# Optimization experiments

Measured on AMD Instinct MI355X. Metric: run time of the kernel, lower is better.

## Reference

```python
import jax, jax.numpy as jnp
import numpy as np

K = 5
K2 = K * K  # 25
SLOPE = 0.01  # torch leaky_relu default


def _unfold(x, k):
    # torch.nn.Unfold(k) on reflect-padded x: channel order c-major, then kh, kw
    b, c, h, w = x.shape
    p = k // 2
    xp = jnp.pad(x, ((0, 0), (0, 0), (p, p), (p, p)), mode='reflect')
    cols = jnp.stack([xp[:, :, i:i + h, j:j + w] for i in range(k) for j in range(k)], axis=2)
    return cols.reshape(b, c * k * k, h * w)  # (b, 3*k^2, h*w)


def _lin(x, W, b):
    # torch Linear: W is (out, in)
    return x @ W.T + b


def _lrelu(x):
    return jnp.where(x >= 0, x, SLOPE * x)


def setup_inputs() -> dict:
    key = jax.random.key(0)
    ks = iter(jax.random.split(key, 64))
    d = {}
    d['x'] = jax.random.uniform(next(ks), (4, 3, 384, 384), dtype=jnp.float32)

    def mk(name, out_f, in_f):
        d['W_' + name] = jax.random.normal(next(ks), (out_f, in_f), jnp.float32) * (1.0 / np.sqrt(in_f))
        d['b_' + name] = jax.random.normal(next(ks), (out_f,), jnp.float32) * 0.01

    mk('input', 2 * K2, 3 * K2)
    mk('h1', 3 * K2, 2 * K2)
    mk('h2', 3 * K2, 3 * K2)
    mk('h3', 2 * K2, 2 * K2)
    mk('h4', 5 * K2, 2 * K2)
    mk('h5', 2 * K2, 5 * K2)
    mk('out', 3, 2 * K2)
    # encoder(3*k^2): in -> 3*in -> in -> 3
    mk('e1', 9 * K2, 3 * K2); mk('e2', 3 * K2, 9 * K2); mk('e3', 3, 3 * K2)
    # encoder(2*k^2)
    mk('f1', 6 * K2, 2 * K2); mk('f2', 2 * K2, 6 * K2); mk('f3', 3, 2 * K2)
    # decoder(2*k^2): 3 -> out -> 3*out -> out
    mk('d1', 2 * K2, 3); mk('d2', 6 * K2, 2 * K2); mk('d3', 2 * K2, 6 * K2)
    return d


def reference(x,
              W_input, b_input, W_h1, b_h1, W_h2, b_h2, W_h3, b_h3,
              W_h4, b_h4, W_h5, b_h5, W_out, b_out,
              W_e1, b_e1, W_e2, b_e2, W_e3, b_e3,
              W_f1, b_f1, W_f2, b_f2, W_f3, b_f3,
              W_d1, b_d1, W_d2, b_d2, W_d3, b_d3):
    b, c, h, w = x.shape
    sw = jnp.transpose(_unfold(x, K), (0, 2, 1))  # (b, h*w, 3*k^2)
    x1 = _lin(sw, W_input, b_input)
    x2 = _lrelu(_lin(x1, W_h1, b_h1))
    x3 = jnp.tanh(_lin(x2, W_h2, b_h2))
    x3_enc = _lin(_lin(_lin(x3, W_e1, b_e1), W_e2, b_e2), W_e3, b_e3)
    enc2_x1 = _lin(_lin(_lin(x1, W_f1, b_f1), W_f2, b_f2), W_f3, b_f3)
    x4 = _lrelu(x3_enc + enc2_x1)
    x4_dec = _lin(_lin(_lin(_lin(x4, W_d1, b_d1), W_d2, b_d2), W_d3, b_d3), W_h3, b_h3)
    x5 = jnp.tanh(_lin(x4_dec, W_h4, b_h4))
    x6 = _lin(x5, W_h5, b_h5) - x1
    x7 = _lrelu(_lin(x6, W_out, b_out))  # (b, h*w, 3)
    return jnp.transpose(x7, (0, 2, 1)).reshape(b, c, h, w)
```

## Files before the change

kernel.cpp:

```cpp
#include <hip/hip_runtime.h>


#define IW 384
#define HW (384 * 384)
#define NPIX (4 * HW)
#define MTILE 128
#define NBLK (NPIX / MTILE)
#define AST 68

typedef _Float16 half8 __attribute__((ext_vector_type(8)));
typedef __fp16 fp16x2 __attribute__((ext_vector_type(2)));
typedef __attribute__((ext_vector_type(4))) float f32x4;
typedef __attribute__((ext_vector_type(4))) unsigned int uint4_;

#define MFMAH(A, B, C) __builtin_amdgcn_mfma_f32_16x16x32_f16((A), (B), (C), 0, 0, 0)

#define BA   0
#define B1   64
#define B2   144
#define BEF  224
#define BD   240
#define B4   304
#define B5   432
#define BOUT 496
#define BIAS_TOT 512

#define W_A0   0
#define W_A1   2048
#define W_A2   4096
#define W_H1A  6144
#define W_H1B  8704
#define W_H2A  11264
#define W_H2B  13824
#define W_H2C  16384
#define W_EF   18944
#define W_D    24064
#define W_H4C0 28160
#define W_H5C0 30208
#define W_OUT  44544
#define W_NI   45568
#define W_TOT  47616

#define STG_BE  24320
#define STG_BF  24336

__device__ __forceinline__ float lrelu(float v) { return v >= 0.0f ? v : 0.01f * v; }

__device__ __forceinline__ float tanh_fast(float v) {
    float e = __expf(2.0f * v);
    return 1.0f - 2.0f * __builtin_amdgcn_rcpf(e + 1.0f);
}

__device__ __forceinline__ unsigned short f2h_bits(float v) {
    union { _Float16 h; unsigned short s; } u; u.h = (_Float16)v; return u.s;
}
__device__ __forceinline__ float h2f_bits(unsigned short s) {
    union { _Float16 h; unsigned short s; } u; u.s = s; return (float)u.h;
}
__device__ __forceinline__ unsigned packh2(float a, float b) {
    union { fp16x2 h; unsigned u; } u;
    u.h = __builtin_amdgcn_cvt_pkrtz(a, b);
    return u.u;
}

__device__ __forceinline__ void stage(float* dst, const float* __restrict__ src,
                                      int n, int tid) {
    int n4 = n >> 2;
    float4* d = (float4*)dst;
    const float4* s = (const float4*)src;
#pragma unroll 4
    for (int i = tid; i < n4; i += 256) d[i] = s[i];
    for (int i = (n4 << 2) + tid; i < n; i += 256) dst[i] = src[i];
}

__global__ __launch_bounds__(256) void setup_all(
    const float* __restrict__ W_input, const float* __restrict__ b_input,
    const float* __restrict__ W_h1,  const float* __restrict__ b_h1,
    const float* __restrict__ W_h2,  const float* __restrict__ b_h2,
    const float* __restrict__ W_h3,  const float* __restrict__ b_h3,
    const float* __restrict__ W_h4,  const float* __restrict__ b_h4,
    const float* __restrict__ W_h5,  const float* __restrict__ b_h5,
    const float* __restrict__ W_out, const float* __restrict__ b_out,
    const float* __restrict__ W_e1,  const float* __restrict__ b_e1,
    const float* __restrict__ W_e2,  const float* __restrict__ b_e2,
    const float* __restrict__ W_e3,  const float* __restrict__ b_e3,
    const float* __restrict__ W_f1,  const float* __restrict__ b_f1,
    const float* __restrict__ W_f2,  const float* __restrict__ b_f2,
    const float* __restrict__ W_f3,  const float* __restrict__ b_f3,
    const float* __restrict__ W_d1,  const float* __restrict__ b_d1,
    const float* __restrict__ W_d2,  const float* __restrict__ b_d2,
    const float* __restrict__ W_d3,  const float* __restrict__ b_d3,
    float* __restrict__ ws)
{
    const int tid = threadIdx.x;
    const int NT = 256;
    short* wimg = (short*)(ws + BIAS_TOT);

    if (blockIdx.x < 71) {
        const int soff[17] = {W_A0,W_A1,W_A2, W_H1A,W_H1B, W_H2A,W_H2B,W_H2C,
                              W_H4C0,W_H5C0, W_H4C0+4096,W_H5C0+4096,
                              W_H4C0+8192,W_H5C0+8192, W_H4C0+12288,W_H5C0+12288,
                              W_OUT};
        const int slay[17] = {0,0,0, 1,1, 2,2,2, 6,7, 6,7, 6,7, 6,7, 8};
        const int sNT[17]  = {4,4,4, 5,5, 5,5,5, 2,4, 2,4, 2,4, 2,4, 1};
        const int sKTS[17] = {1,1,1, 1,1, 1,1,1, 2,1, 2,1, 2,1, 2,1, 2};
        const int snb[17]  = {0,0,0, 0,0, 0,0,0, 0,0, 32,0, 64,0, 96,0, 0};
        const int skb[17]  = {0,32,64, 0,32, 0,32,64, 0,0, 0,32, 0,64, 0,96, 0};

        int seg = 0, local = blockIdx.x;
        while (seg < 16 && local >= sNT[seg] * sKTS[seg]) { local -= sNT[seg] * sKTS[seg]; seg++; }
        const int kts = sKTS[seg];
        const int kt = local % kts, nt = local / kts;
        const int lay = slay[seg];
        short* dst = wimg + soff[seg] + local * 512;

#pragma unroll
        for (int t = 0; t < 2; t++) {
            int idx = tid + t * 256;
            int j = idx & 7, lane = idx >> 3;
            int n = snb[seg] + nt * 16 + (lane & 15);
            int k = skb[seg] + kt * 32 + (lane >> 4) * 8 + j;
            float v = 0.0f;
            switch (lay) {
                case 0: if (n < 50  && k < 75)  v = W_input[n * 75 + k]; break;
                case 1: if (n < 75  && k < 50)  v = W_h1[n * 50 + k]; break;
                case 2: if (n < 75  && k < 75)  v = W_h2[n * 75 + k]; break;
                case 6: if (n < 125 && k < 50)  v = W_h4[n * 50 + k]; break;
                case 7: if (n < 50  && k < 125) v = W_h5[n * 125 + k]; break;
                case 8: if (n < 3   && k < 50)  v = W_out[n * 50 + k]; break;
            }
            dst[idx] = (short)f2h_bits(v);
        }
        return;
    }

    if (blockIdx.x == 74) {
        for (int i = tid; i < BIAS_TOT; i += NT) {
            if (i >= BD && i < B4) continue;
            float v = 0.0f;
            if (i < B1)        { int o = i - BA;   if (o < 50)  v = b_input[o]; }
            else if (i < B2)   { int o = i - B1;   if (o < 75)  v = b_h1[o]; }
            else if (i < BEF)  { int o = i - B2;   if (o < 75)  v = b_h2[o]; }
            else if (i < BD)   { v = 0.0f; }
            else if (i < B5)   { int o = i - B4;   if (o < 125) v = b_h4[o]; }
            else if (i < BOUT) { int o = i - B5;   if (o < 50)  v = b_h5[o]; }
            else               { int o = i - BOUT; if (o < 3)   v = b_out[o]; }
            ws[i] = v;
        }
        for (int i = tid; i < 2048; i += NT) {
            int j = i & 7, lane = (i >> 3) & 63, nt = i >> 9;
            int n = nt * 16 + (lane & 15);
            int k = (nt >> 1) * 32 + (lane >> 4) * 8 + j;
            wimg[W_NI + i] = (short)f2h_bits(k == n ? -1.0f : 0.0f);
        }
        return;
    }

    __shared__ __align__(16) float A[17500];
    __shared__ float B[675];
    __shared__ float C[256];
    __shared__ float Dd[256];
    __shared__ float Es[256];
    __shared__ float S[232];

    if (blockIdx.x == 71) {
        stage(A, W_e2, 16875, tid);
        for (int i = tid; i < 225; i += NT) { Es[i] = W_e3[i]; C[i] = b_e1[i]; }
        __syncthreads();
        for (int o = tid; o < 675; o += NT) {
            int r = o / 225, c = o % 225;
            float s0 = 0.f, s1 = 0.f, s2 = 0.f;
#pragma unroll
            for (int t = 0; t < 75; t += 3) {
                s0 += Es[r * 75 + t]     * A[t * 225 + c];
                s1 += Es[r * 75 + t + 1] * A[(t + 1) * 225 + c];
                s2 += Es[r * 75 + t + 2] * A[(t + 2) * 225 + c];
            }
            B[o] = s0 + s1 + s2;
        }
        for (int o = tid; o < 75; o += NT) {
            float s0 = 0.f, s1 = 0.f, s2 = 0.f;
#pragma unroll
            for (int t = 0; t < 225; t += 3) {
                s0 += A[o * 225 + t]     * C[t];
                s1 += A[o * 225 + t + 1] * C[t + 1];
                s2 += A[o * 225 + t + 2] * C[t + 2];
            }
            Dd[o] = b_e2[o] + s0 + s1 + s2;
        }
        __syncthreads();
        stage(A, W_e1, 16875, tid);
        __syncthreads();
        for (int o = tid; o < 225; o += NT) {
            int r = o / 75, c = o % 75;
            float s0 = 0.f, s1 = 0.f, s2 = 0.f;
#pragma unroll
            for (int t = 0; t < 225; t += 3) {
                s0 += B[r * 225 + t]     * A[t * 75 + c];
                s1 += B[r * 225 + t + 1] * A[(t + 1) * 75 + c];
                s2 += B[r * 225 + t + 2] * A[(t + 2) * 75 + c];
            }
            S[o] = s0 + s1 + s2;
        }
        for (int o = tid; o < 16; o += NT) {
            float s = 0.0f;
            if (o < 3) {
                s = b_e3[o];
                for (int t = 0; t < 75; t++) s += Es[o * 75 + t] * Dd[t];
            }
            ws[STG_BE + o] = s;
        }
        __syncthreads();
        for (int i = tid; i < 3072; i += NT) {
            int j = i & 7, lane = (i >> 3) & 63, frag = i >> 9, pl = frag & 1, kt = frag >> 1;
            int n = lane & 15, k = kt * 32 + (lane >> 4) * 8 + j;
            float v = (n < 3 && k < 75) ? S[n * 75 + k] : 0.0f;
            float hi = h2f_bits(f2h_bits(v));
            wimg[W_EF + i] = (short)(pl ? f2h_bits(v - hi) : f2h_bits(v));
        }
    } else if (blockIdx.x == 72) {
        stage(A,        W_f2, 7500, tid);
        stage(A + 7500, W_f1, 7500, tid);
        for (int i = tid; i < 150; i += NT) { Es[i] = W_f3[i]; C[i] = b_f1[i]; }
        __syncthreads();
        for (int o = tid; o < 450; o += NT) {
            int r = o / 150, c = o % 150;
            float s0 = 0.f, s1 = 0.f;
#pragma unroll
            for (int t = 0; t < 50; t += 2) {
                s0 += Es[r * 50 + t]     * A[t * 150 + c];
                s1 += Es[r * 50 + t + 1] * A[(t + 1) * 150 + c];
            }
            B[o] = s0 + s1;
        }
        for (int o = tid; o < 50; o += NT) {
            float s0 = 0.f, s1 = 0.f;
#pragma unroll
            for (int t = 0; t < 150; t += 2) {
                s0 += A[o * 150 + t]     * C[t];
                s1 += A[o * 150 + t + 1] * C[t + 1];
            }
            Dd[o] = b_f2[o] + s0 + s1;
        }
        __syncthreads();
        for (int o = tid; o < 150; o += NT) {
            int r = o / 50, c = o % 50;
            float s0 = 0.f, s1 = 0.f;
#pragma unroll
            for (int t = 0; t < 150; t += 2) {
                s0 += B[r * 150 + t]     * A[7500 + t * 50 + c];
                s1 += B[r * 150 + t + 1] * A[7500 + (t + 1) * 50 + c];
            }
            S[o] = s0 + s1;
        }
        for (int o = tid; o < 16; o += NT) {
            float s = 0.0f;
            if (o < 3) {
                s = b_f3[o];
                for (int t = 0; t < 50; t++) s += Es[o * 50 + t] * Dd[t];
            }
            ws[STG_BF + o] = s;
        }
        __syncthreads();
        for (int i = tid; i < 2048; i += NT) {
            int j = i & 7, lane = (i >> 3) & 63, frag = i >> 9, pl = frag & 1, kt = frag >> 1;
            int n = lane & 15, k = kt * 32 + (lane >> 4) * 8 + j;
            float v = (n < 3 && k < 50) ? S[n * 50 + k] : 0.0f;
            float hi = h2f_bits(f2h_bits(v));
            wimg[W_EF + 3072 + i] = (short)(pl ? f2h_bits(v - hi) : f2h_bits(v));
        }
    } else {
        stage(A,         W_d2, 7500, tid);
        stage(A + 7500,  W_d3, 7500, tid);
        stage(A + 15000, W_h3, 2500, tid);
        for (int i = tid; i < 150; i += NT) Es[i] = W_d1[i];
        for (int i = tid; i < 50;  i += NT) C[i] = b_d1[i];
        __syncthreads();
        for (int o = tid; o < 450; o += NT) {
            int r = o / 3, c = o % 3;
            float s0 = 0.f, s1 = 0.f;
#pragma unroll
            for (int t = 0; t < 50; t += 2) {
                s0 += A[r * 50 + t]     * Es[t * 3 + c];
                s1 += A[r * 50 + t + 1] * Es[(t + 1) * 3 + c];
            }
            B[o] = s0 + s1;
        }
        for (int o = tid; o < 150; o += NT) {
            float s0 = 0.f, s1 = 0.f;
#pragma unroll
            for (int t = 0; t < 50; t += 2) {
                s0 += A[o * 50 + t]     * C[t];
                s1 += A[o * 50 + t + 1] * C[t + 1];
            }
            Dd[o] = b_d2[o] + s0 + s1;
        }
        __syncthreads();
        for (int o = tid; o < 150; o += NT) {
            int r = o / 3, c = o % 3;
            float s0 = 0.f, s1 = 0.f;
#pragma unroll
            for (int t = 0; t < 150; t += 2) {
                s0 += A[7500 + r * 150 + t]     * B[t * 3 + c];
                s1 += A[7500 + r * 150 + t + 1] * B[(t + 1) * 3 + c];
            }
            Es[o] = s0 + s1;
        }
        for (int o = tid; o < 50; o += NT) {
            float s0 = 0.f, s1 = 0.f;
#pragma unroll
            for (int t = 0; t < 150; t += 2) {
                s0 += A[7500 + o * 150 + t]     * Dd[t];
                s1 += A[7500 + o * 150 + t + 1] * Dd[t + 1];
            }
            C[o] = b_d3[o] + s0 + s1;
        }
        __syncthreads();
        for (int o = tid; o < 150; o += NT) {
            int r = o / 3, c = o % 3;
            float s0 = 0.f, s1 = 0.f;
#pragma unroll
            for (int t = 0; t < 50; t += 2) {
                s0 += A[15000 + r * 50 + t]     * Es[t * 3 + c];
                s1 += A[15000 + r * 50 + t + 1] * Es[(t + 1) * 3 + c];
            }
            S[o] = s0 + s1;
        }
        for (int o = tid; o < 64; o += NT) {
            float v = 0.0f;
            if (o < 50) {
                float s0 = 0.f, s1 = 0.f;
#pragma unroll
                for (int t = 0; t < 50; t += 2) {
                    s0 += A[15000 + o * 50 + t]     * C[t];
                    s1 += A[15000 + o * 50 + t + 1] * C[t + 1];
                }
                v = b_h3[o] + s0 + s1;
            }
            ws[BD + o] = v;
        }
        __syncthreads();
        for (int i = tid; i < 4096; i += NT) {
            int j = i & 7, lane = (i >> 3) & 63, frag = i >> 9, pl = frag & 1, nt = frag >> 1;
            int n = nt * 16 + (lane & 15), k = (lane >> 4) * 8 + j;
            float v = (n < 50 && k < 3) ? S[n * 3 + k] : 0.0f;
            float hi = h2f_bits(f2h_bits(v));
            wimg[W_D + i] = (short)(pl ? f2h_bits(v - hi) : f2h_bits(v));
        }
    }
}

__device__ __forceinline__ half8 gfragH(const short* __restrict__ wl, int off) {
    return *(const half8*)(wl + off);
}

__device__ __forceinline__ half8 readAf(const unsigned int* acts, int row0, int pane, int lane) {
    int m = lane & 15, qd = lane >> 4;
    const unsigned int* p = &acts[(row0 + m) * AST + pane + (qd & 1) * 8];
    uint4_ a = *(const uint4_*)p;
    uint4_ b = *(const uint4_*)(p + 4);
    unsigned sel = (qd >> 1) ? 0x07060302u : 0x05040100u;
    union { unsigned u[4]; half8 v; } r;
    r.u[0] = __builtin_amdgcn_perm(a.y, a.x, sel);
    r.u[1] = __builtin_amdgcn_perm(a.w, a.z, sel);
    r.u[2] = __builtin_amdgcn_perm(b.y, b.x, sel);
    r.u[3] = __builtin_amdgcn_perm(b.w, b.z, sel);
    return r.v;
}

__device__ __forceinline__ void writeCf(unsigned int* acts, int row0q, int dcol,
                                        f32x4 va, f32x4 vb) {
    unsigned int* p = &acts[row0q * AST + dcol];
#pragma unroll
    for (int r = 0; r < 4; r++) p[r * AST] = packh2(va[r], vb[r]);
}

__device__ __forceinline__ void t2s(f32x4& a0, f32x4& a1, half8 x0, half8 x1, half8 b) {
    a0 = MFMAH(x0, b, a0);
    a1 = MFMAH(x1, b, a1);
}
__device__ __forceinline__ void t2p(f32x4& a0, f32x4& a1, half8 x0, half8 x1,
                                    half8 bh, half8 bl) {
    a0 = MFMAH(x0, bh, a0);
    a1 = MFMAH(x1, bh, a1);
    a0 = MFMAH(x0, bl, a0);
    a1 = MFMAH(x1, bl, a1);
}

__global__ __launch_bounds__(256, 4) void fused_mfma(
    const float* __restrict__ xin,
    const float* __restrict__ ws,
    float* __restrict__ out)
{
    __shared__ unsigned int acts[MTILE * AST];

    const int tid = threadIdx.x;
    const int wv = tid >> 6;
    const int lane = tid & 63;
    const int qd = lane >> 4;
    const int mcol = lane & 15;
    const int rw = wv * 32;
    const short* __restrict__ wl = (const short*)(ws + BIAS_TOT) + lane * 8;
    const f32x4 zero4 = {0.f, 0.f, 0.f, 0.f};

    const int g0 = blockIdx.x * MTILE;
    const int bb = g0 / HW;
    const int p0 = g0 - bb * HW;
    const int yb = p0 / IW;
    const int xblk = p0 - yb * IW;
    const float* __restrict__ xb = xin + bb * 3 * HW;

    float* patch = (float*)acts;
    int*   stab  = (int*)(acts + 1984);

    for (int e = tid; e < 1980; e += 256) {
        int cr = e / 132;
        int i  = e - cr * 132;
        int c  = cr / 5, r = cr - c * 5;
        int ty = yb + r - 2; ty = ty < 0 ? -ty : ty; ty = (766 - ty) < ty ? 766 - ty : ty;
        int tx = xblk - 2 + i; tx = tx < 0 ? -tx : tx; tx = (766 - tx) < tx ? 766 - tx : tx;
        patch[cr * 132 + i] = xb[c * HW + ty * IW + tx];
    }
    if (tid < 96) {
        int v = 0;
        if (tid < 75) {
            int c = tid / 25, rem = tid - 25 * c;
            int rr = rem / 5, ss = rem - 5 * rr;
            v = (c * 5 + rr) * 132 + ss;
        }
        stab[tid] = v;
    }
    __syncthreads();

    half8 swf[3][2];
    {
        int st[3][8];
#pragma unroll
        for (int kt = 0; kt < 3; kt++)
#pragma unroll
            for (int j = 0; j < 8; j++)
                st[kt][j] = stab[kt * 32 + qd * 8 + j];
#pragma unroll
        for (int mt = 0; mt < 2; mt++) {
            const int xloc = wv * 32 + mt * 16 + mcol;
#pragma unroll
            for (int kt = 0; kt < 3; kt++) {
                union { unsigned u32[4]; half8 v; } u;
#pragma unroll
                for (int jj = 0; jj < 8; jj += 2) {
                    float v0 = patch[st[kt][jj]     + xloc];
                    float v1 = patch[st[kt][jj + 1] + xloc];
                    if (kt == 2) {
                        int qq0 = 64 + qd * 8 + jj;
                        v0 = (qq0     < 75) ? v0 : 0.0f;
                        v1 = (qq0 + 1 < 75) ? v1 : 0.0f;
                    }
                    u.u32[jj >> 1] = packh2(v0, v1);
                }
                swf[kt][mt] = u.v;
            }
        }
    }
    __syncthreads();

    f32x4 accA[4][2];
#pragma unroll
    for (int nt = 0; nt < 4; nt++) { accA[nt][0] = zero4; accA[nt][1] = zero4; }
#pragma unroll
    for (int nt = 0; nt < 4; nt++)
        t2s(accA[nt][0], accA[nt][1], swf[0][0], swf[0][1], gfragH(wl, W_A0 + nt * 512));
#pragma unroll
    for (int nt = 0; nt < 4; nt++)
        t2s(accA[nt][0], accA[nt][1], swf[1][0], swf[1][1], gfragH(wl, W_A1 + nt * 512));
#pragma unroll
    for (int nt = 0; nt < 4; nt++)
        t2s(accA[nt][0], accA[nt][1], swf[2][0], swf[2][1], gfragH(wl, W_A2 + nt * 512));

    half8 x1f[2][2];
#pragma unroll
    for (int nt = 0; nt < 4; nt++) {
        float bv = ws[BA + nt * 16 + mcol];
#pragma unroll
        for (int mt = 0; mt < 2; mt++) {
            accA[nt][mt][0] += bv; accA[nt][mt][1] += bv;
            accA[nt][mt][2] += bv; accA[nt][mt][3] += bv;
        }
    }
#pragma unroll
    for (int mt = 0; mt < 2; mt++) {
        writeCf(acts, rw + mt * 16 + qd * 4, mcol,      accA[0][mt], accA[1][mt]);
        writeCf(acts, rw + mt * 16 + qd * 4, 16 + mcol, accA[2][mt], accA[3][mt]);
    }
#pragma unroll
    for (int kt = 0; kt < 2; kt++)
#pragma unroll
        for (int mt = 0; mt < 2; mt++)
            x1f[kt][mt] = readAf(acts, rw + mt * 16, kt * 16, lane);

    f32x4 acc1[5][2];
#pragma unroll
    for (int nt = 0; nt < 5; nt++) { acc1[nt][0] = zero4; acc1[nt][1] = zero4; }
#pragma unroll
    for (int nt = 0; nt < 5; nt++)
        t2s(acc1[nt][0], acc1[nt][1], x1f[0][0], x1f[0][1], gfragH(wl, W_H1A + nt * 512));
#pragma unroll
    for (int nt = 0; nt < 5; nt++)
        t2s(acc1[nt][0], acc1[nt][1], x1f[1][0], x1f[1][1], gfragH(wl, W_H1B + nt * 512));
#pragma unroll
    for (int mt = 0; mt < 2; mt++) {
        f32x4 w5[5];
#pragma unroll
        for (int nt = 0; nt < 5; nt++) {
            float bv = ws[B1 + nt * 16 + mcol];
            f32x4 v = acc1[nt][mt];
            v[0] = lrelu(v[0] + bv); v[1] = lrelu(v[1] + bv);
            v[2] = lrelu(v[2] + bv); v[3] = lrelu(v[3] + bv);
            w5[nt] = v;
        }
        writeCf(acts, rw + mt * 16 + qd * 4, mcol,      w5[0], w5[1]);
        writeCf(acts, rw + mt * 16 + qd * 4, 16 + mcol, w5[2], w5[3]);
        writeCf(acts, rw + mt * 16 + qd * 4, 32 + mcol, w5[4], zero4);
    }

    f32x4 acc2[5][2];
#pragma unroll
    for (int nt = 0; nt < 5; nt++) { acc2[nt][0] = zero4; acc2[nt][1] = zero4; }
    {
        half8 a0 = readAf(acts, rw, 0, lane), a1 = readAf(acts, rw + 16, 0, lane);
#pragma unroll
        for (int nt = 0; nt < 5; nt++)
            t2s(acc2[nt][0], acc2[nt][1], a0, a1, gfragH(wl, W_H2A + nt * 512));
    }
    {
        half8 a0 = readAf(acts, rw, 16, lane), a1 = readAf(acts, rw + 16, 16, lane);
#pragma unroll
        for (int nt = 0; nt < 5; nt++)
            t2s(acc2[nt][0], acc2[nt][1], a0, a1, gfragH(wl, W_H2B + nt * 512));
    }
    {
        half8 a0 = readAf(acts, rw, 32, lane), a1 = readAf(acts, rw + 16, 32, lane);
#pragma unroll
        for (int nt = 0; nt < 5; nt++)
            t2s(acc2[nt][0], acc2[nt][1], a0, a1, gfragH(wl, W_H2C + nt * 512));
    }
#pragma unroll
    for (int mt = 0; mt < 2; mt++) {
        f32x4 w5[5];
#pragma unroll
        for (int nt = 0; nt < 5; nt++) {
            float bv = ws[B2 + nt * 16 + mcol];
            f32x4 v = acc2[nt][mt];
            v[0] = tanh_fast(v[0] + bv); v[1] = tanh_fast(v[1] + bv);
            v[2] = tanh_fast(v[2] + bv); v[3] = tanh_fast(v[3] + bv);
            w5[nt] = v;
        }
        writeCf(acts, rw + mt * 16 + qd * 4, mcol,      w5[0], w5[1]);
        writeCf(acts, rw + mt * 16 + qd * 4, 16 + mcol, w5[2], w5[3]);
        writeCf(acts, rw + mt * 16 + qd * 4, 32 + mcol, w5[4], zero4);
    }

    f32x4 accEF[2];
    {
        float bv = ws[STG_BE + mcol] + ws[STG_BF + mcol];
        accEF[0] = (f32x4){bv, bv, bv, bv};
        accEF[1] = accEF[0];
    }
#pragma unroll
    for (int kt = 0; kt < 3; kt++) {
        half8 a0 = readAf(acts, rw, kt * 16, lane), a1 = readAf(acts, rw + 16, kt * 16, lane);
        t2p(accEF[0], accEF[1], a0, a1,
            gfragH(wl, W_EF + kt * 1024), gfragH(wl, W_EF + kt * 1024 + 512));
    }
#pragma unroll
    for (int kt = 0; kt < 2; kt++)
        t2p(accEF[0], accEF[1], x1f[kt][0], x1f[kt][1],
            gfragH(wl, W_EF + 3072 + kt * 1024), gfragH(wl, W_EF + 3072 + kt * 1024 + 512));
    half8 x4f[2];
#pragma unroll
    for (int mt = 0; mt < 2; mt++) {
        f32x4 v = accEF[mt];
        v[0] = lrelu(v[0]); v[1] = lrelu(v[1]); v[2] = lrelu(v[2]); v[3] = lrelu(v[3]);
        writeCf(acts, rw + mt * 16 + qd * 4, 32 + mcol, v, zero4);
    }
    x4f[0] = readAf(acts, rw, 32, lane);
    x4f[1] = readAf(acts, rw + 16, 32, lane);

    f32x4 accD[4][2];
#pragma unroll
    for (int nt = 0; nt < 4; nt++) {
        float bv = ws[BD + nt * 16 + mcol];
        accD[nt][0] = (f32x4){bv, bv, bv, bv};
        accD[nt][1] = accD[nt][0];
    }
#pragma unroll
    for (int nt = 0; nt < 4; nt++)
        t2p(accD[nt][0], accD[nt][1], x4f[0], x4f[1],
            gfragH(wl, W_D + nt * 1024), gfragH(wl, W_D + nt * 1024 + 512));
#pragma unroll
    for (int mt = 0; mt < 2; mt++) {
        writeCf(acts, rw + mt * 16 + qd * 4, mcol,      accD[0][mt], accD[1][mt]);
        writeCf(acts, rw + mt * 16 + qd * 4, 16 + mcol, accD[2][mt], accD[3][mt]);
    }
    half8 xdf[2][2];
#pragma unroll
    for (int kt = 0; kt < 2; kt++)
#pragma unroll
        for (int mt = 0; mt < 2; mt++)
            xdf[kt][mt] = readAf(acts, rw + mt * 16, kt * 16, lane);

    f32x4 x6a[4][2];
#pragma unroll
    for (int nt = 0; nt < 4; nt++) {
        float bv = ws[B5 + nt * 16 + mcol];
        half8 nI = gfragH(wl, W_NI + nt * 512);
#pragma unroll
        for (int mt = 0; mt < 2; mt++) {
            f32x4 v = {bv, bv, bv, bv};
            x6a[nt][mt] = MFMAH(x1f[nt >> 1][mt], nI, v);
        }
    }

#pragma unroll
    for (int c = 0; c < 4; c++) {
        const int slot = 32 + (c & 1) * 16;
        f32x4 acc5[2][2];
#pragma unroll
        for (int nt2 = 0; nt2 < 2; nt2++) {
            float bv = ws[B4 + c * 32 + nt2 * 16 + mcol];
            acc5[nt2][0] = (f32x4){bv, bv, bv, bv};
            acc5[nt2][1] = acc5[nt2][0];
        }
#pragma unroll
        for (int nt2 = 0; nt2 < 2; nt2++)
#pragma unroll
            for (int kt = 0; kt < 2; kt++)
                t2s(acc5[nt2][0], acc5[nt2][1], xdf[kt][0], xdf[kt][1],
                    gfragH(wl, W_H4C0 + c * 4096 + (nt2 * 2 + kt) * 512));
#pragma unroll
        for (int mt = 0; mt < 2; mt++) {
            f32x4 v0 = acc5[0][mt], v1 = acc5[1][mt];
            v0[0] = tanh_fast(v0[0]); v0[1] = tanh_fast(v0[1]);
            v0[2] = tanh_fast(v0[2]); v0[3] = tanh_fast(v0[3]);
            v1[0] = tanh_fast(v1[0]); v1[1] = tanh_fast(v1[1]);
            v1[2] = tanh_fast(v1[2]); v1[3] = tanh_fast(v1[3]);
            writeCf(acts, rw + mt * 16 + qd * 4, slot + mcol, v0, v1);
        }
        half8 chf[2];
        chf[0] = readAf(acts, rw, slot, lane);
        chf[1] = readAf(acts, rw + 16, slot, lane);
#pragma unroll
        for (int nt = 0; nt < 4; nt++)
            t2s(x6a[nt][0], x6a[nt][1], chf[0], chf[1],
                gfragH(wl, W_H5C0 + c * 4096 + nt * 512));
    }

#pragma unroll
    for (int mt = 0; mt < 2; mt++) {
        writeCf(acts, rw + mt * 16 + qd * 4, mcol,      x6a[0][mt], x6a[1][mt]);
        writeCf(acts, rw + mt * 16 + qd * 4, 16 + mcol, x6a[2][mt], x6a[3][mt]);
    }
    f32x4 accO[2];
    {
        float bv = ws[BOUT + mcol];
        accO[0] = (f32x4){bv, bv, bv, bv};
        accO[1] = accO[0];
    }
#pragma unroll
    for (int kt = 0; kt < 2; kt++) {
        half8 a0 = readAf(acts, rw, kt * 16, lane), a1 = readAf(acts, rw + 16, kt * 16, lane);
        t2s(accO[0], accO[1], a0, a1, gfragH(wl, W_OUT + kt * 512));
    }
    if (mcol < 3) {
#pragma unroll
        for (int mt = 0; mt < 2; mt++) {
#pragma unroll
            for (int r = 0; r < 4; r++) {
                int p = p0 + wv * 32 + mt * 16 + qd * 4 + r;
                out[(bb * 3 + mcol) * HW + p] = lrelu(accO[mt][r]);
            }
        }
    }
}

extern "C" void kernel_launch(void* const* d_in, const int* in_sizes, int n_in,
                              void* d_out, int out_size, void* d_ws, size_t ws_size,
                              hipStream_t stream)
{
    const float* xin = (const float*)d_in[0];
    float* ws = (float*)d_ws;

    setup_all<<<75, 256, 0, stream>>>(
        (const float*)d_in[1],  (const float*)d_in[2],
        (const float*)d_in[3],  (const float*)d_in[4],
        (const float*)d_in[5],  (const float*)d_in[6],
        (const float*)d_in[7],  (const float*)d_in[8],
        (const float*)d_in[9],  (const float*)d_in[10],
        (const float*)d_in[11], (const float*)d_in[12],
        (const float*)d_in[13], (const float*)d_in[14],
        (const float*)d_in[15], (const float*)d_in[16],
        (const float*)d_in[17], (const float*)d_in[18],
        (const float*)d_in[19], (const float*)d_in[20],
        (const float*)d_in[21], (const float*)d_in[22],
        (const float*)d_in[23], (const float*)d_in[24],
        (const float*)d_in[25], (const float*)d_in[26],
        (const float*)d_in[27], (const float*)d_in[28],
        (const float*)d_in[29], (const float*)d_in[30],
        (const float*)d_in[31], (const float*)d_in[32],
        ws);

    fused_mfma<<<NBLK, 256, 0, stream>>>(xin, ws, (float*)d_out);
}
```

Before: 226.5 us.

## Transpose MFMA operand roles so activations round-trip LDS with vector stores

Swaps the MFMA operand order so weights are the A operand and pixel activations the B operand. Each lane then owns contiguous output features for one pixel, which lets intermediate activations be written as packed 64-bit stores and read back as 128-bit loads without byte permutes. Biases are loaded as vectors into the accumulator initialisation, the LDS row stride shrinks, and occupancy hints rise to 6 blocks. tanh now uses exp2 with a folded constant and lrelu uses fmax. This relies on the weight image layout being valid for the transposed operand role, and on padding being zeroed correctly after the masking for the third K tile was removed.

```diff
diff --git a/kernel.cpp b/kernel.cpp
--- a/kernel.cpp
+++ b/kernel.cpp
@@ -6,12 +6,13 @@
 #define NPIX (4 * HW)
 #define MTILE 128
 #define NBLK (NPIX / MTILE)
-#define AST 68
+#define NST 52
+#define PT16 (16 * NST)
 
 typedef _Float16 half8 __attribute__((ext_vector_type(8)));
 typedef __fp16 fp16x2 __attribute__((ext_vector_type(2)));
 typedef __attribute__((ext_vector_type(4))) float f32x4;
-typedef __attribute__((ext_vector_type(4))) unsigned int uint4_;
+typedef __attribute__((ext_vector_type(2))) unsigned int uint2_;
 
 #define MFMAH(A, B, C) __builtin_amdgcn_mfma_f32_16x16x32_f16((A), (B), (C), 0, 0, 0)
 
@@ -44,11 +45,17 @@
 #define STG_BE  24320
 #define STG_BF  24336
 
-__device__ __forceinline__ float lrelu(float v) { return v >= 0.0f ? v : 0.01f * v; }
+__device__ __forceinline__ float lrelu(float v) { return fmaxf(v, 0.01f * v); }
+
+#if __has_builtin(__builtin_amdgcn_exp2f)
+#define EXP2F __builtin_amdgcn_exp2f
+#else
+#define EXP2F __builtin_exp2f
+#endif
 
 __device__ __forceinline__ float tanh_fast(float v) {
-    float e = __expf(2.0f * v);
-    return 1.0f - 2.0f * __builtin_amdgcn_rcpf(e + 1.0f);
+    float e = EXP2F(v * 2.8853900817779268f);
+    return __builtin_fmaf(-2.0f, __builtin_amdgcn_rcpf(e + 1.0f), 1.0f);
 }
 
 __device__ __forceinline__ unsigned short f2h_bits(float v) {
@@ -354,54 +361,36 @@
     return *(const half8*)(wl + off);
 }
 
-__device__ __forceinline__ half8 readAf(const unsigned int* acts, int row0, int pane, int lane) {
-    int m = lane & 15, qd = lane >> 4;
-    const unsigned int* p = &acts[(row0 + m) * AST + pane + (qd & 1) * 8];
-    uint4_ a = *(const uint4_*)p;
-    uint4_ b = *(const uint4_*)(p + 4);
-    unsigned sel = (qd >> 1) ? 0x07060302u : 0x05040100u;
-    union { unsigned u[4]; half8 v; } r;
-    r.u[0] = __builtin_amdgcn_perm(a.y, a.x, sel);
-    r.u[1] = __builtin_amdgcn_perm(a.w, a.z, sel);
-    r.u[2] = __builtin_amdgcn_perm(b.y, b.x, sel);
-    r.u[3] = __builtin_amdgcn_perm(b.w, b.z, sel);
-    return r.v;
-}
-
-__device__ __forceinline__ void writeCf(unsigned int* acts, int row0q, int dcol,
-                                        f32x4 va, f32x4 vb) {
-    unsigned int* p = &acts[row0q * AST + dcol];
-#pragma unroll
-    for (int r = 0; r < 4; r++) p[r * AST] = packh2(va[r], vb[r]);
-}
-
-__device__ __forceinline__ void t2s(f32x4& a0, f32x4& a1, half8 x0, half8 x1, half8 b) {
-    a0 = MFMAH(x0, b, a0);
-    a1 = MFMAH(x1, b, a1);
-}
-__device__ __forceinline__ void t2p(f32x4& a0, f32x4& a1, half8 x0, half8 x1,
-                                    half8 bh, half8 bl) {
-    a0 = MFMAH(x0, bh, a0);
-    a1 = MFMAH(x1, bh, a1);
-    a0 = MFMAH(x0, bl, a0);
-    a1 = MFMAH(x1, bl, a1);
-}
-
-__global__ __launch_bounds__(256, 4) void fused_mfma(
+__device__ __forceinline__ void wB(unsigned int* p, f32x4 v) {
+    uint2_ u;
+    u[0] = packh2(v[0], v[1]);
+    u[1] = packh2(v[2], v[3]);
+    *(uint2_*)p = u;
+}
+
+__device__ __forceinline__ f32x4 lrelu4(f32x4 v) {
+    v[0] = lrelu(v[0]); v[1] = lrelu(v[1]); v[2] = lrelu(v[2]); v[3] = lrelu(v[3]);
+    return v;
+}
+__device__ __forceinline__ f32x4 tanh4(f32x4 v) {
+    v[0] = tanh_fast(v[0]); v[1] = tanh_fast(v[1]);
+    v[2] = tanh_fast(v[2]); v[3] = tanh_fast(v[3]);
+    return v;
+}
+
+__global__ __launch_bounds__(256, 6) void fused_mfma(
     const float* __restrict__ xin,
     const float* __restrict__ ws,
     float* __restrict__ out)
 {
-    __shared__ unsigned int acts[MTILE * AST];
+    __shared__ unsigned int acts[MTILE * NST];
 
     const int tid = threadIdx.x;
     const int wv = tid >> 6;
     const int lane = tid & 63;
     const int qd = lane >> 4;
     const int mcol = lane & 15;
-    const int rw = wv * 32;
     const short* __restrict__ wl = (const short*)(ws + BIAS_TOT) + lane * 8;
-    const f32x4 zero4 = {0.f, 0.f, 0.f, 0.f};
 
     const int g0 = blockIdx.x * MTILE;
     const int bb = g0 / HW;
@@ -441,8 +430,8 @@
             for (int j = 0; j < 8; j++)
                 st[kt][j] = stab[kt * 32 + qd * 8 + j];
 #pragma unroll
-        for (int mt = 0; mt < 2; mt++) {
-            const int xloc = wv * 32 + mt * 16 + mcol;
+        for (int pt = 0; pt < 2; pt++) {
+            const int xloc = wv * 32 + pt * 16 + mcol;
 #pragma unroll
             for (int kt = 0; kt < 3; kt++) {
                 union { unsigned u32[4]; half8 v; } u;
@@ -450,234 +439,213 @@
                 for (int jj = 0; jj < 8; jj += 2) {
                     float v0 = patch[st[kt][jj]     + xloc];
                     float v1 = patch[st[kt][jj + 1] + xloc];
-                    if (kt == 2) {
-                        int qq0 = 64 + qd * 8 + jj;
-                        v0 = (qq0     < 75) ? v0 : 0.0f;
-                        v1 = (qq0 + 1 < 75) ? v1 : 0.0f;
-                    }
                     u.u32[jj >> 1] = packh2(v0, v1);
                 }
-                swf[kt][mt] = u.v;
+                swf[kt][pt] = u.v;
             }
         }
     }
     __syncthreads();
 
+    unsigned int* myrow = acts + (wv * 32 + mcol) * NST;
+    unsigned int* wp = myrow + 2 * qd;
+    const unsigned int* rp = myrow + 4 * qd;
+
+    {
+        uint2_ z; z[0] = 0u; z[1] = 0u;
+        *(uint2_*)(wp + 40) = z;
+        *(uint2_*)(wp + PT16 + 40) = z;
+    }
+
     f32x4 accA[4][2];
 #pragma unroll
-    for (int nt = 0; nt < 4; nt++) { accA[nt][0] = zero4; accA[nt][1] = zero4; }
-#pragma unroll
-    for (int nt = 0; nt < 4; nt++)
-        t2s(accA[nt][0], accA[nt][1], swf[0][0], swf[0][1], gfragH(wl, W_A0 + nt * 512));
-#pragma unroll
-    for (int nt = 0; nt < 4; nt++)
-        t2s(accA[nt][0], accA[nt][1], swf[1][0], swf[1][1], gfragH(wl, W_A1 + nt * 512));
-#pragma unroll
-    for (int nt = 0; nt < 4; nt++)
-        t2s(accA[nt][0], accA[nt][1], swf[2][0], swf[2][1], gfragH(wl, W_A2 + nt * 512));
-
+    for (int mt = 0; mt < 4; mt++) {
+        f32x4 b = *(const f32x4*)(ws + BA + mt * 16 + qd * 4);
+        accA[mt][0] = b; accA[mt][1] = b;
+    }
+#pragma unroll
+    for (int kt = 0; kt < 3; kt++)
+#pragma unroll
+        for (int mt = 0; mt < 4; mt++) {
+            half8 w = gfragH(wl, W_A0 + kt * 2048 + mt * 512);
+            accA[mt][0] = MFMAH(w, swf[kt][0], accA[mt][0]);
+            accA[mt][1] = MFMAH(w, swf[kt][1], accA[mt][1]);
+        }
+#pragma unroll
+    for (int mt = 0; mt < 4; mt++) {
+        wB(wp + mt * 8,        accA[mt][0]);
+        wB(wp + PT16 + mt * 8, accA[mt][1]);
+    }
     half8 x1f[2][2];
 #pragma unroll
-    for (int nt = 0; nt < 4; nt++) {
-        float bv = ws[BA + nt * 16 + mcol];
-#pragma unroll
-        for (int mt = 0; mt < 2; mt++) {
-            accA[nt][mt][0] += bv; accA[nt][mt][1] += bv;
-            accA[nt][mt][2] += bv; accA[nt][mt][3] += bv;
-        }
-    }
-#pragma unroll
-    for (int mt = 0; mt < 2; mt++) {
-        writeCf(acts, rw + mt * 16 + qd * 4, mcol,      accA[0][mt], accA[1][mt]);
-        writeCf(acts, rw + mt * 16 + qd * 4, 16 + mcol, accA[2][mt], accA[3][mt]);
+    for (int kt = 0; kt < 2; kt++) {
+        x1f[kt][0] = *(const half8*)(rp + kt * 16);
+        x1f[kt][1] = *(const half8*)(rp + PT16 + kt * 16);
+    }
+
+    f32x4 acc1[5][2];
+#pragma unroll
+    for (int mt = 0; mt < 5; mt++) {
+        f32x4 b = *(const f32x4*)(ws + B1 + mt * 16 + qd * 4);
+        acc1[mt][0] = b; acc1[mt][1] = b;
     }
 #pragma unroll
     for (int kt = 0; kt < 2; kt++)
 #pragma unroll
-        for (int mt = 0; mt < 2; mt++)
-            x1f[kt][mt] = readAf(acts, rw + mt * 16, kt * 16, lane);
-
-    f32x4 acc1[5][2];
-#pragma unroll
-    for (int nt = 0; nt < 5; nt++) { acc1[nt][0] = zero4; acc1[nt][1] = zero4; }
-#pragma unroll
-    for (int nt = 0; nt < 5; nt++)
-        t2s(acc1[nt][0], acc1[nt][1], x1f[0][0], x1f[0][1], gfragH(wl, W_H1A + nt * 512));
-#pragma unroll
-    for (int nt = 0; nt < 5; nt++)
-        t2s(acc1[nt][0], acc1[nt][1], x1f[1][0], x1f[1][1], gfragH(wl, W_H1B + nt * 512));
-#pragma unroll
-    for (int mt = 0; mt < 2; mt++) {
-        f32x4 w5[5];
-#pragma unroll
-        for (int nt = 0; nt < 5; nt++) {
-            float bv = ws[B1 + nt * 16 + mcol];
-            f32x4 v = acc1[nt][mt];
-            v[0] = lrelu(v[0] + bv); v[1] = lrelu(v[1] + bv);
-            v[2] = lrelu(v[2] + bv); v[3] = lrelu(v[3] + bv);
-            w5[nt] = v;
-        }
-        writeCf(acts, rw + mt * 16 + qd * 4, mcol,      w5[0], w5[1]);
-        writeCf(acts, rw + mt * 16 + qd * 4, 16 + mcol, w5[2], w5[3]);
-        writeCf(acts, rw + mt * 16 + qd * 4, 32 + mcol, w5[4], zero4);
+        for (int mt = 0; mt < 5; mt++) {
+            half8 w = gfragH(wl, W_H1A + kt * 2560 + mt * 512);
+            acc1[mt][0] = MFMAH(w, x1f[kt][0], acc1[mt][0]);
+            acc1[mt][1] = MFMAH(w, x1f[kt][1], acc1[mt][1]);
+        }
+#pragma unroll
+    for (int mt = 0; mt < 5; mt++) {
+        wB(wp + mt * 8,        lrelu4(acc1[mt][0]));
+        wB(wp + PT16 + mt * 8, lrelu4(acc1[mt][1]));
     }
 
     f32x4 acc2[5][2];
 #pragma unroll
-    for (int nt = 0; nt < 5; nt++) { acc2[nt][0] = zero4; acc2[nt][1] = zero4; }
-    {
-        half8 a0 = readAf(acts, rw, 0, lane), a1 = readAf(acts, rw + 16, 0, lane);
-#pragma unroll
-        for (int nt = 0; nt < 5; nt++)
-            t2s(acc2[nt][0], acc2[nt][1], a0, a1, gfragH(wl, W_H2A + nt * 512));
-    }
-    {
-        half8 a0 = readAf(acts, rw, 16, lane), a1 = readAf(acts, rw + 16, 16, lane);
-#pragma unroll
-        for (int nt = 0; nt < 5; nt++)
-            t2s(acc2[nt][0], acc2[nt][1], a0, a1, gfragH(wl, W_H2B + nt * 512));
-    }
-    {
-        half8 a0 = readAf(acts, rw, 32, lane), a1 = readAf(acts, rw + 16, 32, lane);
-#pragma unroll
-        for (int nt = 0; nt < 5; nt++)
-            t2s(acc2[nt][0], acc2[nt][1], a0, a1, gfragH(wl, W_H2C + nt * 512));
-    }
-#pragma unroll
-    for (int mt = 0; mt < 2; mt++) {
-        f32x4 w5[5];
-#pragma unroll
-        for (int nt = 0; nt < 5; nt++) {
-            float bv = ws[B2 + nt * 16 + mcol];
-            f32x4 v = acc2[nt][mt];
-            v[0] = tanh_fast(v[0] + bv); v[1] = tanh_fast(v[1] + bv);
-            v[2] = tanh_fast(v[2] + bv); v[3] = tanh_fast(v[3] + bv);
-            w5[nt] = v;
-        }
-        writeCf(acts, rw + mt * 16 + qd * 4, mcol,      w5[0], w5[1]);
-        writeCf(acts, rw + mt * 16 + qd * 4, 16 + mcol, w5[2], w5[3]);
-        writeCf(acts, rw + mt * 16 + qd * 4, 32 + mcol, w5[4], zero4);
+    for (int mt = 0; mt < 5; mt++) {
+        f32x4 b = *(const f32x4*)(ws + B2 + mt * 16 + qd * 4);
+        acc2[mt][0] = b; acc2[mt][1] = b;
+    }
+#pragma unroll
+    for (int kt = 0; kt < 3; kt++) {
+        half8 a0 = *(const half8*)(rp + kt * 16);
+        half8 a1 = *(const half8*)(rp + PT16 + kt * 16);
+#pragma unroll
+        for (int mt = 0; mt < 5; mt++) {
+            half8 w = gfragH(wl, W_H2A + kt * 2560 + mt * 512);
+            acc2[mt][0] = MFMAH(w, a0, acc2[mt][0]);
+            acc2[mt][1] = MFMAH(w, a1, acc2[mt][1]);
+        }
+    }
+#pragma unroll
+    for (int mt = 0; mt < 5; mt++) {
+        wB(wp + mt * 8,        tanh4(acc2[mt][0]));
+        wB(wp + PT16 + mt * 8, tanh4(acc2[mt][1]));
     }
 
     f32x4 accEF[2];
     {
-        float bv = ws[STG_BE + mcol] + ws[STG_BF + mcol];
-        accEF[0] = (f32x4){bv, bv, bv, bv};
-        accEF[1] = accEF[0];
+        f32x4 be = *(const f32x4*)(ws + STG_BE + qd * 4);
+        f32x4 bf = *(const f32x4*)(ws + STG_BF + qd * 4);
+        f32x4 b = be + bf;
+        accEF[0] = b; accEF[1] = b;
     }
 #pragma unroll
     for (int kt = 0; kt < 3; kt++) {
-        half8 a0 = readAf(acts, rw, kt * 16, lane), a1 = readAf(acts, rw + 16, kt * 16, lane);
-        t2p(accEF[0], accEF[1], a0, a1,
-            gfragH(wl, W_EF + kt * 1024), gfragH(wl, W_EF + kt * 1024 + 512));
-    }
-#pragma unroll
-    for (int kt = 0; kt < 2; kt++)
-        t2p(accEF[0], accEF[1], x1f[kt][0], x1f[kt][1],
-            gfragH(wl, W_EF + 3072 + kt * 1024), gfragH(wl, W_EF + 3072 + kt * 1024 + 512));
+        half8 a0 = *(const half8*)(rp + kt * 16);
+        half8 a1 = *(const half8*)(rp + PT16 + kt * 16);
+        half8 wh = gfragH(wl, W_EF + kt * 1024);
+        half8 wo = gfragH(wl, W_EF + kt * 1024 + 512);
+        accEF[0] = MFMAH(wh, a0, accEF[0]); accEF[0] = MFMAH(wo, a0, accEF[0]);
+        accEF[1] = MFMAH(wh, a1, accEF[1]); accEF[1] = MFMAH(wo, a1, accEF[1]);
+    }
+#pragma unroll
+    for (int kt = 0; kt < 2; kt++) {
+        half8 wh = gfragH(wl, W_EF + 3072 + kt * 1024);
+        half8 wo = gfragH(wl, W_EF + 3072 + kt * 1024 + 512);
+        accEF[0] = MFMAH(wh, x1f[kt][0], accEF[0]); accEF[0] = MFMAH(wo, x1f[kt][0], accEF[0]);
+        accEF[1] = MFMAH(wh, x1f[kt][1], accEF[1]); accEF[1] = MFMAH(wo, x1f[kt][1], accEF[1]);
+    }
+    wB(wp,        lrelu4(accEF[0]));
+    wB(wp + PT16, lrelu4(accEF[1]));
+
     half8 x4f[2];
-#pragma unroll
-    for (int mt = 0; mt < 2; mt++) {
-        f32x4 v = accEF[mt];
-        v[0] = lrelu(v[0]); v[1] = lrelu(v[1]); v[2] = lrelu(v[2]); v[3] = lrelu(v[3]);
-        writeCf(acts, rw + mt * 16 + qd * 4, 32 + mcol, v, zero4);
-    }
-    x4f[0] = readAf(acts, rw, 32, lane);
-    x4f[1] = readAf(acts, rw + 16, 32, lane);
-
+    x4f[0] = *(const half8*)(rp);
+    x4f[1] = *(const half8*)(rp + PT16);
     f32x4 accD[4][2];
 #pragma unroll
-    for (int nt = 0; nt < 4; nt++) {
-        float bv = ws[BD + nt * 16 + mcol];
-        accD[nt][0] = (f32x4){bv, bv, bv, bv};
-        accD[nt][1] = accD[nt][0];
-    }
-#pragma unroll
-    for (int nt = 0; nt < 4; nt++)
-        t2p(accD[nt][0], accD[nt][1], x4f[0], x4f[1],
-            gfragH(wl, W_D + nt * 1024), gfragH(wl, W_D + nt * 1024 + 512));
-#pragma unroll
-    for (int mt = 0; mt < 2; mt++) {
-        writeCf(acts, rw + mt * 16 + qd * 4, mcol,      accD[0][mt], accD[1][mt]);
-        writeCf(acts, rw + mt * 16 + qd * 4, 16 + mcol, accD[2][mt], accD[3][mt]);
+    for (int mt = 0; mt < 4; mt++) {
+        f32x4 b = *(const f32x4*)(ws + BD + mt * 16 + qd * 4);
+        accD[mt][0] = b; accD[mt][1] = b;
+    }
+#pragma unroll
+    for (int mt = 0; mt < 4; mt++) {
+        half8 wh = gfragH(wl, W_D + mt * 1024);
+        half8 wo = gfragH(wl, W_D + mt * 1024 + 512);
+        accD[mt][0] = MFMAH(wh, x4f[0], accD[mt][0]); accD[mt][0] = MFMAH(wo, x4f[0], accD[mt][0]);
+        accD[mt][1] = MFMAH(wh, x4f[1], accD[mt][1]); accD[mt][1] = MFMAH(wo, x4f[1], accD[mt][1]);
+    }
+#pragma unroll
+    for (int mt = 0; mt < 4; mt++) {
+        wB(wp + mt * 8,        accD[mt][0]);
+        wB(wp + PT16 + mt * 8, accD[mt][1]);
     }
     half8 xdf[2][2];
 #pragma unroll
-    for (int kt = 0; kt < 2; kt++)
-#pragma unroll
-        for (int mt = 0; mt < 2; mt++)
-            xdf[kt][mt] = readAf(acts, rw + mt * 16, kt * 16, lane);
+    for (int kt = 0; kt < 2; kt++) {
+        xdf[kt][0] = *(const half8*)(rp + kt * 16);
+        xdf[kt][1] = *(const half8*)(rp + PT16 + kt * 16);
+    }
 
     f32x4 x6a[4][2];
 #pragma unroll
-    for (int nt = 0; nt < 4; nt++) {
-        float bv = ws[B5 + nt * 16 + mcol];
-        half8 nI = gfragH(wl, W_NI + nt * 512);
-#pragma unroll
-        for (int mt = 0; mt < 2; mt++) {
-            f32x4 v = {bv, bv, bv, bv};
-            x6a[nt][mt] = MFMAH(x1f[nt >> 1][mt], nI, v);
-        }
+    for (int mt = 0; mt < 4; mt++) {
+        f32x4 b = *(const f32x4*)(ws + B5 + mt * 16 + qd * 4);
+        half8 nI = gfragH(wl, W_NI + mt * 512);
+        x6a[mt][0] = MFMAH(nI, x1f[mt >> 1][0], b);
+        x6a[mt][1] = MFMAH(nI, x1f[mt >> 1][1], b);
     }
 
 #pragma unroll
     for (int c = 0; c < 4; c++) {
-        const int slot = 32 + (c & 1) * 16;
+        const int slot = (c & 1) ? 16 : 32;
         f32x4 acc5[2][2];
 #pragma unroll
-        for (int nt2 = 0; nt2 < 2; nt2++) {
-            float bv = ws[B4 + c * 32 + nt2 * 16 + mcol];
-            acc5[nt2][0] = (f32x4){bv, bv, bv, bv};
-            acc5[nt2][1] = acc5[nt2][0];
-        }
-#pragma unroll
-        for (int nt2 = 0; nt2 < 2; nt2++)
-#pragma unroll
-            for (int kt = 0; kt < 2; kt++)
-                t2s(acc5[nt2][0], acc5[nt2][1], xdf[kt][0], xdf[kt][1],
-                    gfragH(wl, W_H4C0 + c * 4096 + (nt2 * 2 + kt) * 512));
-#pragma unroll
-        for (int mt = 0; mt < 2; mt++) {
-            f32x4 v0 = acc5[0][mt], v1 = acc5[1][mt];
-            v0[0] = tanh_fast(v0[0]); v0[1] = tanh_fast(v0[1]);
-            v0[2] = tanh_fast(v0[2]); v0[3] = tanh_fast(v0[3]);
-            v1[0] = tanh_fast(v1[0]); v1[1] = tanh_fast(v1[1]);
-            v1[2] = tanh_fast(v1[2]); v1[3] = tanh_fast(v1[3]);
-            writeCf(acts, rw + mt * 16 + qd * 4, slot + mcol, v0, v1);
-        }
-        half8 chf[2];
-        chf[0] = readAf(acts, rw, slot, lane);
-        chf[1] = readAf(acts, rw + 16, slot, lane);
-#pragma unroll
-        for (int nt = 0; nt < 4; nt++)
-            t2s(x6a[nt][0], x6a[nt][1], chf[0], chf[1],
-                gfragH(wl, W_H5C0 + c * 4096 + nt * 512));
-    }
-
-#pragma unroll
-    for (int mt = 0; mt < 2; mt++) {
-        writeCf(acts, rw + mt * 16 + qd * 4, mcol,      x6a[0][mt], x6a[1][mt]);
-        writeCf(acts, rw + mt * 16 + qd * 4, 16 + mcol, x6a[2][mt], x6a[3][mt]);
+        for (int mt2 = 0; mt2 < 2; mt2++) {
+            f32x4 b = *(const f32x4*)(ws + B4 + c * 32 + mt2 * 16 + qd * 4);
+            acc5[mt2][0] = b; acc5[mt2][1] = b;
+        }
+#pragma unroll
+        for (int kt = 0; kt < 2; kt++)
+#pragma unroll
+            for (int mt2 = 0; mt2 < 2; mt2++) {
+                half8 w = gfragH(wl, W_H4C0 + c * 4096 + (mt2 * 2 + kt) * 512);
+                acc5[mt2][0] = MFMAH(w, xdf[kt][0], acc5[mt2][0]);
+                acc5[mt2][1] = MFMAH(w, xdf[kt][1], acc5[mt2][1]);
+            }
+#pragma unroll
+        for (int mt2 = 0; mt2 < 2; mt2++) {
+            wB(wp + slot + mt2 * 8,        tanh4(acc5[mt2][0]));
+            wB(wp + PT16 + slot + mt2 * 8, tanh4(acc5[mt2][1]));
+        }
+        half8 ch0 = *(const half8*)(rp + slot);
+        half8 ch1 = *(const half8*)(rp + PT16 + slot);
+#pragma unroll
+        for (int mt = 0; mt < 4; mt++) {
+            half8 w = gfragH(wl, W_H5C0 + c * 4096 + mt * 512);
+            x6a[mt][0] = MFMAH(w, ch0, x6a[mt][0]);
+            x6a[mt][1] = MFMAH(w, ch1, x6a[mt][1]);
+        }
+    }
+
+#pragma unroll
+    for (int mt = 0; mt < 4; mt++) {
+        wB(wp + mt * 8,        x6a[mt][0]);
+        wB(wp + PT16 + mt * 8, x6a[mt][1]);
     }
     f32x4 accO[2];
     {
-        float bv = ws[BOUT + mcol];
-        accO[0] = (f32x4){bv, bv, bv, bv};
-        accO[1] = accO[0];
+        f32x4 b = *(const f32x4*)(ws + BOUT + qd * 4);
+        accO[0] = b; accO[1] = b;
     }
 #pragma unroll
     for (int kt = 0; kt < 2; kt++) {
-        half8 a0 = readAf(acts, rw, kt * 16, lane), a1 = readAf(acts, rw + 16, kt * 16, lane);
-        t2s(accO[0], accO[1], a0, a1, gfragH(wl, W_OUT + kt * 512));
-    }
-    if (mcol < 3) {
-#pragma unroll
-        for (int mt = 0; mt < 2; mt++) {
-#pragma unroll
-            for (int r = 0; r < 4; r++) {
-                int p = p0 + wv * 32 + mt * 16 + qd * 4 + r;
-                out[(bb * 3 + mcol) * HW + p] = lrelu(accO[mt][r]);
-            }
+        half8 a0 = *(const half8*)(rp + kt * 16);
+        half8 a1 = *(const half8*)(rp + PT16 + kt * 16);
+        half8 w = gfragH(wl, W_OUT + kt * 512);
+        accO[0] = MFMAH(w, a0, accO[0]);
+        accO[1] = MFMAH(w, a1, accO[1]);
+    }
+    if (qd == 0) {
+#pragma unroll
+        for (int pt = 0; pt < 2; pt++) {
+            int p = p0 + wv * 32 + pt * 16 + mcol;
+#pragma unroll
+            for (int r = 0; r < 3; r++)
+                out[(bb * 3 + r) * HW + p] = lrelu(accO[pt][r]);
         }
     }
 }
```

Result: slower. 244.6 us (+8.0%).
